# Kernel optimization log

Measured on AMD Instinct MI355X. Metric: run time of the kernel, lower is better.

Reference implementation:

```python
import jax, jax.numpy as jnp
import numpy as np

B, S, D, F, E, CAP = 4, 2048, 1024, 4096, 8, 320


def setup_inputs() -> dict:
    key = jax.random.key(0)
    k1, k2, k3, k4 = jax.random.split(key, 4)
    return {
        "hidden_states": jax.random.normal(k1, (B, S, D), dtype=jnp.float32),
        "router_w": jax.random.normal(k2, (D, E), dtype=jnp.float32) * 0.02,
        "wi": jax.random.normal(k3, (E, D, F), dtype=jnp.float32) * 0.02,
        "wo": jax.random.normal(k4, (E, F, D), dtype=jnp.float32) * 0.02,
    }


def reference(hidden_states, router_w, wi, wo):
    # ---- Router (Switch top-1 with per-sequence expert capacity) ----
    b, s, d = hidden_states.shape
    e = router_w.shape[1]
    logits = hidden_states.astype(jnp.float32) @ router_w          # [B,S,E]
    probs = jax.nn.softmax(logits, axis=-1)                        # [B,S,E]
    expert_idx = jnp.argmax(probs, axis=-1)                        # [B,S]
    onehot = jax.nn.one_hot(expert_idx, e, dtype=jnp.int32)        # [B,S,E]
    priority = jnp.cumsum(onehot, axis=1)                          # cumsum over seq dim (dim=-2)
    keep = onehot * (priority <= CAP).astype(jnp.int32)            # capacity-masked router_mask

    # slot of each token within its chosen expert (0-based)
    slot = jnp.take_along_axis(priority, expert_idx[..., None], axis=-1)[..., 0] - 1  # [B,S]
    valid = slot < CAP                                             # dropped tokens exceed capacity
    slot_sc = jnp.where(valid, slot, CAP)                          # out-of-range -> dropped by scatter

    b_ar = jnp.broadcast_to(jnp.arange(b)[:, None], (b, s))
    s_ar = jnp.broadcast_to(jnp.arange(s)[None, :], (b, s))
    dispatch = jnp.zeros((b, e, CAP), jnp.int32).at[b_ar, expert_idx, slot_sc].set(
        s_ar.astype(jnp.int32), mode="drop")                       # [B,E,CAP] token index per slot
    slot_used = jnp.zeros((b, e, CAP), bool).at[b_ar, expert_idx, slot_sc].set(
        valid, mode="drop")                                        # [B,E,CAP]

    # ---- Dispatch: gather tokens into [B,E,CAP,D] ----
    xg = jax.vmap(lambda xb, ib: xb[ib])(hidden_states, dispatch)  # [B,E,CAP,D]

    # ---- Per-expert dense FFN (grouped GEMM) ----
    hg = jax.nn.relu(jnp.einsum("becd,edf->becf", xg, wi))         # [B,E,CAP,F]
    yg = jnp.einsum("becf,efd->becd", hg, wo)                      # [B,E,CAP,D]

    # ---- Combine: scatter expert outputs back; unrouted tokens keep input ----
    idx_back = jnp.where(slot_used, dispatch, s)                   # out-of-range -> dropped
    next_states = jax.vmap(
        lambda xb, ib, yb: xb.at[ib.reshape(-1)].set(yb.reshape(-1, d), mode="drop")
    )(hidden_states, idx_back, yg)                                 # [B,S,D]

    max_prob = jnp.max(probs, axis=-1, keepdims=True)              # [B,S,1]
    out = max_prob * next_states
    expert_index_out = jnp.argmax(keep, axis=-1)                   # [B,S] (0 for dropped tokens)
    return out, logits, expert_index_out
```

## Files before the change

kernel.cpp:

```cpp
#include <hip/hip_runtime.h>
#include <hip/hip_bf16.h>
#include <stdint.h>

#define B_ 4
#define S_ 2048
#define D_ 1024
#define F_ 4096
#define E_ 8
#define CAP_ 320
#define BS_ (B_*S_)
#define MPE 1280

typedef unsigned short u16;
typedef __attribute__((ext_vector_type(8))) short bf16x8;
typedef __attribute__((ext_vector_type(4))) float f32x4;
typedef __attribute__((ext_vector_type(4))) unsigned short u16x4;
typedef __attribute__((ext_vector_type(8))) unsigned short u16x8;

__device__ __forceinline__ u16 f2bf(float f) {
  union { float f; uint32_t u; } v; v.f = f;
  uint32_t r = (v.u + 0x7FFFu + ((v.u >> 16) & 1u)) >> 16;
  return (u16)r;
}

__device__ __forceinline__ void gload16(const void* g, void* l) {
  __builtin_amdgcn_global_load_lds(
      (const __attribute__((address_space(1))) uint32_t*)g,
      (__attribute__((address_space(3))) uint32_t*)l, 16, 0, 0);
}

__device__ __forceinline__ void transpose_block(
    const float* __restrict__ W, u16* __restrict__ WT,
    const int K, const int N, const int bid, void* ldsraw)
{
  float (*tile)[65] = (float(*)[65])ldsraw;
  const int tk = K >> 7, tn = N >> 6;
  const int e = bid / (tk * tn), r = bid % (tk * tn);
  const int k0 = (r / tn) << 7, n0 = (r % tn) << 6;
  const float* We = W + (size_t)e * K * N;
  u16* WTe = WT + (size_t)e * N * K;
  const int t = threadIdx.x;
  const int fr = t >> 2, c0 = (t & 3) * 16;
#pragma unroll
  for (int j = 0; j < 4; ++j) {
    const float4 v = *(const float4*)(We + (size_t)(k0 + fr) * N + n0 + c0 + j * 4);
    tile[fr][c0 + j*4 + 0] = v.x; tile[fr][c0 + j*4 + 1] = v.y;
    tile[fr][c0 + j*4 + 2] = v.z; tile[fr][c0 + j*4 + 3] = v.w;
  }
  __syncthreads();
  const int nr = t >> 3, kk0 = (t & 7) * 16;
  u16x8 o0, o1;
#pragma unroll
  for (int j = 0; j < 8; ++j) o0[j] = f2bf(tile[kk0 + j][nr]);
#pragma unroll
  for (int j = 0; j < 8; ++j) o1[j] = f2bf(tile[kk0 + 8 + j][nr]);
  u16* dst = WTe + (size_t)(n0 + nr) * K + k0 + kk0;
  *(u16x8*)dst = o0;
  *(u16x8*)(dst + 8) = o1;
}

__global__ __launch_bounds__(512) void transpose_kernel(
    const float* __restrict__ W, u16* __restrict__ WT, const int K, const int N)
{
  __shared__ __align__(16) float tile[128][65];
  transpose_block(W, WT, K, N, blockIdx.x, (void*)tile);
}

__global__ __launch_bounds__(512) void prep_kernel(
    const float* __restrict__ hs, const float* __restrict__ rw,
    const float* __restrict__ wi, u16* __restrict__ wT,
    float* __restrict__ logits, float* __restrict__ maxp,
    int* __restrict__ eidx, const int twiT)
{
  __shared__ __align__(16) float tile[128][65];
  if ((int)blockIdx.x < twiT) {
    transpose_block(wi, wT, D_, F_, blockIdx.x, (void*)tile);
    return;
  }
  const int wv = threadIdx.x >> 6, l = threadIdx.x & 63;
  const int token = (blockIdx.x - twiT) * 8 + wv;
  const float* row = hs + (size_t)token * D_;
  const float4* rw4 = (const float4*)rw;

  double acc0=0, acc1=0, acc2=0, acc3=0, acc4=0, acc5=0, acc6=0, acc7=0;
#pragma unroll
  for (int j = 0; j < 4; ++j) {
    const int d4 = l + j * 64;
    const float4 v = ((const float4*)row)[d4];
#pragma unroll
    for (int c = 0; c < 4; ++c) {
      const int d = d4 * 4 + c;
      const float x = (&v.x)[c];
      const float4 w0 = rw4[d * 2];
      const float4 w1 = rw4[d * 2 + 1];
      acc0 += (double)x * (double)w0.x;
      acc1 += (double)x * (double)w0.y;
      acc2 += (double)x * (double)w0.z;
      acc3 += (double)x * (double)w0.w;
      acc4 += (double)x * (double)w1.x;
      acc5 += (double)x * (double)w1.y;
      acc6 += (double)x * (double)w1.z;
      acc7 += (double)x * (double)w1.w;
    }
  }
  double acc[E_] = {acc0, acc1, acc2, acc3, acc4, acc5, acc6, acc7};
#pragma unroll
  for (int e = 0; e < E_; ++e) {
#pragma unroll
    for (int off = 32; off; off >>= 1)
      acc[e] += __shfl_xor(acc[e], off);
  }
  if (l == 0) {
    float lg[E_];
#pragma unroll
    for (int e = 0; e < E_; ++e) lg[e] = (float)acc[e];
    float lmax = lg[0]; int am = 0;
#pragma unroll
    for (int e = 1; e < E_; ++e) { if (lg[e] > lmax) { lmax = lg[e]; am = e; } }
    float sum = 0.f;
#pragma unroll
    for (int e = 0; e < E_; ++e) sum += expf(lg[e] - lmax);
#pragma unroll
    for (int e = 0; e < E_; ++e) logits[(size_t)token * E_ + e] = lg[e];
    maxp[token] = 1.0f / sum;
    eidx[token] = am;
  }
}

__global__ __launch_bounds__(256) void scan_kernel(
    const int* __restrict__ eidx, int* __restrict__ tok,
    float* __restrict__ eout, const float* __restrict__ hs,
    const float* __restrict__ maxp, float* __restrict__ out)
{
  const int b = blockIdx.x >> 3, e = blockIdx.x & 7;
  __shared__ int wsum[4];
  const int tid = threadIdx.x, wv = tid >> 6, l = tid & 63;
  for (int i = tid; i < CAP_; i += 256) tok[(b * E_ + e) * CAP_ + i] = -1;
  __syncthreads();
  int base = 0;
  for (int ch = 0; ch < S_ / 256; ++ch) {
    const int s = ch * 256 + tid;
    const bool p = (eidx[b * S_ + s] == e);
    const unsigned long long m = __ballot(p);
    const int lp = __popcll(m & ((1ULL << l) - 1ULL));
    if (l == 0) wsum[wv] = __popcll(m);
    __syncthreads();
    int pre = 0, tot = 0;
#pragma unroll
    for (int w = 0; w < 4; ++w) { if (w < wv) pre += wsum[w]; tot += wsum[w]; }
    if (p) {
      const int rank = base + pre + lp;
      if (rank < CAP_) {
        tok[(b * E_ + e) * CAP_ + rank] = s;
        eout[b * S_ + s] = (float)e;
      } else {
        eout[b * S_ + s] = 0.0f;
        const float mp = maxp[b * S_ + s];
        const float4* src = (const float4*)(hs + (size_t)(b * S_ + s) * D_);
        float4* dst = (float4*)(out + (size_t)(b * S_ + s) * D_);
        for (int j = 0; j < D_ / 4; ++j) {
          const float4 vv = src[j];
          float4 o; o.x = vv.x * mp; o.y = vv.y * mp; o.z = vv.z * mp; o.w = vv.w * mp;
          dst[j] = o;
        }
      }
    }
    base += tot;
    __syncthreads();
  }
}

__global__ __launch_bounds__(256) void gather_kernel(
    const float* __restrict__ hs, const int* __restrict__ tok,
    u16* __restrict__ Xg)
{
  const int bx = blockIdx.x;
  const int e = bx / MPE, r = bx % MPE;
  const int b = r / CAP_, c = r % CAP_;
  const int t = tok[(b * E_ + e) * CAP_ + c];
  const int d = threadIdx.x * 4;
  u16x4 o;
  if (t >= 0) {
    const float4 vv = *(const float4*)(hs + ((size_t)(b * S_ + t)) * D_ + d);
    o[0] = f2bf(vv.x); o[1] = f2bf(vv.y); o[2] = f2bf(vv.z); o[3] = f2bf(vv.w);
  } else {
    o[0] = 0; o[1] = 0; o[2] = 0; o[3] = 0;
  }
  *(u16x4*)(Xg + (size_t)bx * D_ + d) = o;
}

#define BAR() __builtin_amdgcn_s_barrier()
#define VMW(n) asm volatile("s_waitcnt vmcnt(" #n ")" ::: "memory")

__global__ __launch_bounds__(512, 2) void moe_g1(
    const u16* __restrict__ Aall, const u16* __restrict__ Btall,
    u16* __restrict__ hgout, const int gemm_blocks,
    const float* __restrict__ Wtr, u16* __restrict__ WTtr)
{
  __shared__ __align__(16) u16 lds[49152];

#define LDA(p, h) (lds + (p) * 8192 + (h) * 4096)
#define LDB(p, h) (lds + 16384 + (p) * 16384 + (h) * 8192)

  if ((int)blockIdx.x >= gemm_blocks) {
    transpose_block(Wtr, WTtr, F_, D_, blockIdx.x - gemm_blocks, (void*)lds);
    return;
  }
  const int K = D_, NT = K >> 6, N = F_;
  const int cpx = gemm_blocks >> 3;
  const int bid = blockIdx.x;
  const int swzb = (bid & 7) * cpx + (bid >> 3);
  const int e = swzb / 160, rem = swzb % 160;
  const int m0 = (rem % 10) * 128, n0 = (rem / 10) * 256;

  const u16* Ae = Aall + (size_t)e * MPE * K;
  const u16* Be = Btall + (size_t)e * N * K;

  const int tid = threadIdx.x;
  const int wv = tid >> 6, l = tid & 63;
  const int wr = wv >> 2, wc = wv & 3;
  const int lr = l & 15, lk = l >> 4;
  const int rswz = ((lr >> 3) & 1) << 4;
  const int gs0 = tid ^ (((tid >> 5) & 1) << 1);
  const size_t goffB = (size_t)((gs0 >> 2) & 127) * K + (size_t)((gs0 & 3) * 8);
  const size_t goffA = (size_t)((gs0 >> 2) & 63) * K
                     + (size_t)(((gs0 >> 8) & 1) * 32) + (size_t)((gs0 & 3) * 8);
  const int dwoff = wv * 512;

  const u16* pA0 = Ae + (size_t)m0 * K;
  const u16* pA1 = Ae + (size_t)(m0 + 64) * K;
  const u16* pB0 = Be + (size_t)n0 * K;
  const u16* pB1 = Be + (size_t)(n0 + 128) * K;

  f32x4 acc[4][4];
#pragma unroll
  for (int i = 0; i < 4; ++i)
#pragma unroll
    for (int j = 0; j < 4; ++j) acc[i][j] = (f32x4){0.f, 0.f, 0.f, 0.f};

  bf16x8 faA[2], faB[2], fb[8];

#define STAGE_A1(dhalf, rb, tt) \
    gload16((rb) + goffA + (size_t)((tt) * 64), (dhalf) + dwoff)

#define STAGE_B1(dhalf, rb, tt) do {                                       \
    const u16* s_ = (rb) + goffB + (size_t)((tt) * 64);                    \
    gload16(s_,      (dhalf) + dwoff);                                     \
    gload16(s_ + 32, (dhalf) + 4096 + dwoff);                              \
  } while (0)

#define READ_AQ1(q, p, fa_) do {                                           \
    _Pragma("unroll")                                                      \
    for (int kk = 0; kk < 2; ++kk)                                         \
      fa_[kk] = *(const bf16x8*)&LDA(p, wr)                                \
          [(kk*64 + (q)*16 + lr)*32 + ((lk*8) ^ rswz)];                    \
  } while (0)

#define READ_B_ALL1(p) do {                                                \
    _Pragma("unroll")                                                      \
    for (int nf = 0; nf < 4; ++nf)                                         \
      _Pragma("unroll")                                                    \
      for (int kk = 0; kk < 2; ++kk)                                       \
        fb[nf*2+kk] = *(const bf16x8*)&LDB(p, wc>>1)                       \
            [(kk*128 + (wc&1)*64 + (nf>>1)*32 + (nf&1)*16 + lr)*32         \
             + ((lk*8) ^ rswz)];                                           \
  } while (0)

#define MFMA_P1(q, fa_) do {                                               \
    __builtin_amdgcn_s_setprio(1);                                         \
    _Pragma("unroll")                                                      \
    for (int nf = 0; nf < 4; ++nf)                                         \
      _Pragma("unroll")                                                    \
      for (int kk = 0; kk < 2; ++kk)                                       \
        acc[q][nf] = __builtin_amdgcn_mfma_f32_16x16x32_bf16(              \
            fa_[kk], fb[nf*2+kk], acc[q][nf], 0, 0, 0);                    \
    __builtin_amdgcn_s_setprio(0);                                         \
  } while (0)

#define DO_T1(p, pn, tc) do {                                              \
    READ_AQ1(1, p, faB);                                                   \
    if ((tc) + 1 < NT) { STAGE_A1(LDA(pn,0), pA0, (tc)+1);                 \
                         STAGE_A1(LDA(pn,1), pA1, (tc)+1); }               \
    MFMA_P1(0, faA);                                                       \
    READ_AQ1(2, p, faA);                                                   \
    MFMA_P1(1, faB);                                                       \
    BAR();                                                                 \
    READ_AQ1(3, p, faB);                                                   \
    if ((tc) + 2 < NT) { STAGE_B1(LDB(p,0), pB0, (tc)+2);                  \
                         STAGE_B1(LDB(p,1), pB1, (tc)+2); }                \
    MFMA_P1(2, faA);                                                       \
    MFMA_P1(3, faB);                                                       \
    if ((tc) >= NT - 2) VMW(0); else VMW(4);                               \
    BAR();                                                                 \
    if ((tc) + 1 < NT) { READ_B_ALL1(pn); READ_AQ1(0, pn, faA); }          \
  } while (0)

  STAGE_A1(LDA(0,0), pA0, 0);
  STAGE_A1(LDA(0,1), pA1, 0);
  STAGE_B1(LDB(0,0), pB0, 0);
  STAGE_B1(LDB(0,1), pB1, 0);
  STAGE_B1(LDB(1,0), pB0, 1);
  STAGE_B1(LDB(1,1), pB1, 1);
  VMW(4); BAR();
  READ_B_ALL1(0); READ_AQ1(0, 0, faA);

  for (int t = 0; t < NT; t += 2) {
    DO_T1(0, 1, t);
    DO_T1(1, 0, t + 1);
  }

#pragma unroll
  for (int i = 0; i < 4; ++i) {
#pragma unroll
    for (int r = 0; r < 4; ++r) {
      const int grow = m0 + wr * 64 + i * 16 + lk * 4 + r;
      u16* hrow = hgout + ((size_t)e * MPE + grow) * (size_t)N + n0 + wc * 64;
#pragma unroll
      for (int j = 0; j < 4; ++j)
        hrow[j * 16 + lr] = f2bf(fmaxf(acc[i][j][r], 0.0f));
    }
  }
#undef LDA
#undef LDB
#undef STAGE_A1
#undef STAGE_B1
#undef READ_AQ1
#undef READ_B_ALL1
#undef MFMA_P1
#undef DO_T1
}

__global__ __launch_bounds__(512, 2) void moe_g2(
    const u16* __restrict__ Aall, const u16* __restrict__ Btall,
    float* __restrict__ out, const int* __restrict__ tok,
    const float* __restrict__ maxp)
{
  __shared__ __align__(16) u16 lds[2][2][2][8192];

  const int K = F_, NT = K >> 6, N = D_;
  const int gemm_blocks = 160, cpx = gemm_blocks >> 3;
  const int bid = blockIdx.x;
  const int swzb = (bid & 7) * cpx + (bid >> 3);
  const int e = swzb / 20, rem = swzb % 20;
  const int m0 = (rem % 5) * 256, n0 = (rem / 5) * 256;

  const u16* Ae = Aall + (size_t)e * MPE * K;
  const u16* Be = Btall + (size_t)e * N * K;

  const int tid = threadIdx.x;
  const int wv = tid >> 6, l = tid & 63;
  const int wr = wv >> 2, wc = wv & 3;
  const int lr = l & 15, lk = l >> 4;
  const int rswz = ((lr >> 3) & 1) << 4;
  const int gs0 = tid ^ (((tid >> 5) & 1) << 1);
  const size_t goff = (size_t)((gs0 >> 2) & 127) * K + (size_t)((gs0 & 3) * 8);
  const int dwoff = wv * 512;

  const u16* pA0 = Ae + (size_t)m0 * K;
  const u16* pA1 = Ae + (size_t)(m0 + 128) * K;
  const u16* pB0 = Be + (size_t)n0 * K;
  const u16* pB1 = Be + (size_t)(n0 + 128) * K;

  f32x4 acc[8][4];
#pragma unroll
  for (int i = 0; i < 8; ++i)
#pragma unroll
    for (int j = 0; j < 4; ++j) acc[i][j] = (f32x4){0.f, 0.f, 0.f, 0.f};

  bf16x8 faA[4], faB[4], fb[8];

#define LDSH(p, ab, h) (&lds[p][ab][h][0])

#define STAGE2(dhalf, rb, tt) do {                                         \
    const u16* s_ = (rb) + goff + (size_t)((tt) * 64);                     \
    gload16(s_,      (dhalf) + dwoff);                                     \
    gload16(s_ + 32, (dhalf) + 4096 + dwoff);                              \
  } while (0)

#define READ_AQ2(q, p, fa_) do {                                           \
    _Pragma("unroll")                                                      \
    for (int mf = 0; mf < 2; ++mf)                                         \
      _Pragma("unroll")                                                    \
      for (int kk = 0; kk < 2; ++kk)                                       \
        fa_[mf*2+kk] = *(const bf16x8*)&lds[p][0][wr]                      \
            [(kk*128 + (q)*32 + mf*16 + lr)*32 + ((lk*8) ^ rswz)];         \
  } while (0)

#define READ_B_ALL2(p) do {                                                \
    _Pragma("unroll")                                                      \
    for (int nf = 0; nf < 4; ++nf)                                         \
      _Pragma("unroll")                                                    \
      for (int kk = 0; kk < 2; ++kk)                                       \
        fb[nf*2+kk] = *(const bf16x8*)&lds[p][1][wc>>1]                    \
            [(kk*128 + (wc&1)*64 + (nf>>1)*32 + (nf&1)*16 + lr)*32         \
             + ((lk*8) ^ rswz)];                                           \
  } while (0)

#define MFMA_P2(q, fa_) do {                                               \
    __builtin_amdgcn_s_setprio(1);                                         \
    _Pragma("unroll")                                                      \
    for (int mf = 0; mf < 2; ++mf)                                         \
      _Pragma("unroll")                                                    \
      for (int nf = 0; nf < 4; ++nf)                                       \
        _Pragma("unroll")                                                  \
        for (int kk = 0; kk < 2; ++kk)                                     \
          acc[(q)*2+mf][nf] = __builtin_amdgcn_mfma_f32_16x16x32_bf16(     \
              fa_[mf*2+kk], fb[nf*2+kk], acc[(q)*2+mf][nf], 0, 0, 0);      \
    __builtin_amdgcn_s_setprio(0);                                         \
  } while (0)

#define DO_T2(p, pn, tc) do {                                              \
    READ_AQ2(1, p, faB);                                                   \
    if ((tc) + 1 < NT) { STAGE2(LDSH(pn,0,0), pA0, (tc)+1);                \
                         STAGE2(LDSH(pn,0,1), pA1, (tc)+1); }              \
    MFMA_P2(0, faA);                                                       \
    READ_AQ2(2, p, faA);                                                   \
    MFMA_P2(1, faB);                                                       \
    BAR();                                                                 \
    READ_AQ2(3, p, faB);                                                   \
    if ((tc) + 2 < NT) { STAGE2(LDSH(p,1,0), pB0, (tc)+2);                 \
                         STAGE2(LDSH(p,1,1), pB1, (tc)+2); }               \
    MFMA_P2(2, faA);                                                       \
    MFMA_P2(3, faB);                                                       \
    if ((tc) >= NT - 2) VMW(0); else VMW(4);                               \
    BAR();                                                                 \
    if ((tc) + 1 < NT) { READ_B_ALL2(pn); READ_AQ2(0, pn, faA); }          \
  } while (0)

  STAGE2(LDSH(0,0,0), pA0, 0);
  STAGE2(LDSH(0,0,1), pA1, 0);
  STAGE2(LDSH(0,1,0), pB0, 0);
  STAGE2(LDSH(0,1,1), pB1, 0);
  STAGE2(LDSH(1,1,0), pB0, 1);
  STAGE2(LDSH(1,1,1), pB1, 1);
  VMW(4); BAR();
  READ_B_ALL2(0); READ_AQ2(0, 0, faA);

  for (int t = 0; t < NT; t += 2) {
    DO_T2(0, 1, t);
    DO_T2(1, 0, t + 1);
  }

#pragma unroll
  for (int i = 0; i < 8; ++i) {
#pragma unroll
    for (int r = 0; r < 4; ++r) {
      const int grow = m0 + wr * 128 + i * 16 + lk * 4 + r;
      const int b = grow / CAP_, c = grow % CAP_;
      const int t = tok[(b * E_ + e) * CAP_ + c];
      if (t >= 0) {
        const float sc = maxp[b * S_ + t];
        float* orow = out + ((size_t)(b * S_ + t)) * D_ + n0 + wc * 64;
#pragma unroll
        for (int j = 0; j < 4; ++j)
          orow[j * 16 + lr] = sc * acc[i][j][r];
      }
    }
  }
#undef LDSH
#undef STAGE2
#undef READ_AQ2
#undef READ_B_ALL2
#undef MFMA_P2
#undef DO_T2
}

extern "C" void kernel_launch(void* const* d_in, const int* in_sizes, int n_in,
                              void* d_out, int out_size, void* d_ws, size_t ws_size,
                              hipStream_t stream)
{
  const float* hs = (const float*)d_in[0];
  const float* rw = (const float*)d_in[1];
  const float* wi = (const float*)d_in[2];
  const float* wo = (const float*)d_in[3];

  float* out    = (float*)d_out;
  float* logits = out + (size_t)BS_ * D_;
  float* eout   = logits + (size_t)BS_ * E_;

  uint8_t* ws = (uint8_t*)d_ws;
  int*   tok  = (int*)(ws + 0);
  float* maxp = (float*)(ws + 40960);
  int*   eidx = (int*)(ws + 73728);
  u16*   Xg   = (u16*)(ws + 131072);
  u16*   hg   = (u16*)(ws + 21102592);
  u16*   wiT  = (u16*)(ws + 104988672);
  if (ws_size < 172097536ULL) return;
  const bool big = ws_size >= 239206400ULL;
  u16* woT = big ? (u16*)(ws + 172097536) : wiT;

  const int twiT = E_ * (D_ / 128) * (F_ / 64);
  const int twoT = E_ * (F_ / 128) * (D_ / 64);
  const int g1 = E_ * (MPE / 128) * (F_ / 256);
  const int g2 = 160;

  prep_kernel<<<twiT + BS_ / 8, 512, 0, stream>>>(
      hs, rw, wi, wiT, logits, maxp, eidx, twiT);
  scan_kernel<<<B_ * E_, 256, 0, stream>>>(eidx, tok, eout, hs, maxp, out);
  gather_kernel<<<E_ * MPE, 256, 0, stream>>>(hs, tok, Xg);

  if (big) {
    moe_g1<<<g1 + twoT, 512, 0, stream>>>(Xg, wiT, hg, g1, wo, woT);
  } else {
    moe_g1<<<g1, 512, 0, stream>>>(Xg, wiT, hg, g1, nullptr, nullptr);
    transpose_kernel<<<twoT, 512, 0, stream>>>(wo, woT, F_, D_);
  }
  moe_g2<<<g2, 512, 0, stream>>>(hg, woT, out, tok, maxp);
}
```

Before: 326.4 us.

## Single-buffer B tile in first grouped GEMM to cut LDS usage

The B operand in the first expert GEMM goes from double-buffered to a single LDS buffer, shrinking shared memory from 96KB to 64KB per block. The prefetch of B now runs one tile ahead instead of two. Each step waits for all global loads to finish and adds an extra barrier after the register reads from LDS. The aim is to lower LDS pressure, possibly to allow more resident blocks, at the cost of a shallower pipeline and extra synchronisation per K-step.

```diff
diff --git a/kernel.cpp b/kernel.cpp
--- a/kernel.cpp
+++ b/kernel.cpp
@@ -190,6 +190,7 @@
 }
 
 #define BAR() __builtin_amdgcn_s_barrier()
+#define LGKM0() asm volatile("s_waitcnt lgkmcnt(0)" ::: "memory")
 #define VMW(n) asm volatile("s_waitcnt vmcnt(" #n ")" ::: "memory")
 
 __global__ __launch_bounds__(512, 2) void moe_g1(
@@ -197,10 +198,10 @@
     u16* __restrict__ hgout, const int gemm_blocks,
     const float* __restrict__ Wtr, u16* __restrict__ WTtr)
 {
-  __shared__ __align__(16) u16 lds[49152];
+  __shared__ __align__(16) u16 lds[32768];
 
 #define LDA(p, h) (lds + (p) * 8192 + (h) * 4096)
-#define LDB(p, h) (lds + 16384 + (p) * 16384 + (h) * 8192)
+#define LDB(h)    (lds + 16384 + (h) * 8192)
 
   if ((int)blockIdx.x >= gemm_blocks) {
     transpose_block(Wtr, WTtr, F_, D_, blockIdx.x - gemm_blocks, (void*)lds);
@@ -256,12 +257,12 @@
           [(kk*64 + (q)*16 + lr)*32 + ((lk*8) ^ rswz)];                    \
   } while (0)
 
-#define READ_B_ALL1(p) do {                                                \
+#define READ_B_ALL1() do {                                                 \
     _Pragma("unroll")                                                      \
     for (int nf = 0; nf < 4; ++nf)                                         \
       _Pragma("unroll")                                                    \
       for (int kk = 0; kk < 2; ++kk)                                       \
-        fb[nf*2+kk] = *(const bf16x8*)&LDB(p, wc>>1)                       \
+        fb[nf*2+kk] = *(const bf16x8*)&LDB(wc>>1)                          \
             [(kk*128 + (wc&1)*64 + (nf>>1)*32 + (nf&1)*16 + lr)*32         \
              + ((lk*8) ^ rswz)];                                           \
   } while (0)
@@ -278,31 +279,33 @@
   } while (0)
 
 #define DO_T1(p, pn, tc) do {                                              \
+    if ((tc) + 1 < NT) {                                                   \
+      STAGE_A1(LDA(pn,0), pA0, (tc)+1);                                    \
+      STAGE_A1(LDA(pn,1), pA1, (tc)+1);                                    \
+      STAGE_B1(LDB(0), pB0, (tc)+1);                                       \
+      STAGE_B1(LDB(1), pB1, (tc)+1);                                       \
+    }                                                                      \
     READ_AQ1(1, p, faB);                                                   \
-    if ((tc) + 1 < NT) { STAGE_A1(LDA(pn,0), pA0, (tc)+1);                 \
-                         STAGE_A1(LDA(pn,1), pA1, (tc)+1); }               \
     MFMA_P1(0, faA);                                                       \
     READ_AQ1(2, p, faA);                                                   \
     MFMA_P1(1, faB);                                                       \
-    BAR();                                                                 \
     READ_AQ1(3, p, faB);                                                   \
-    if ((tc) + 2 < NT) { STAGE_B1(LDB(p,0), pB0, (tc)+2);                  \
-                         STAGE_B1(LDB(p,1), pB1, (tc)+2); }                \
     MFMA_P1(2, faA);                                                       \
     MFMA_P1(3, faB);                                                       \
-    if ((tc) >= NT - 2) VMW(0); else VMW(4);                               \
+    VMW(0);                                                                \
     BAR();                                                                 \
-    if ((tc) + 1 < NT) { READ_B_ALL1(pn); READ_AQ1(0, pn, faA); }          \
+    if ((tc) + 1 < NT) { READ_B_ALL1(); READ_AQ1(0, pn, faA); }            \
+    LGKM0();                                                               \
+    BAR();                                                                 \
   } while (0)
 
   STAGE_A1(LDA(0,0), pA0, 0);
   STAGE_A1(LDA(0,1), pA1, 0);
-  STAGE_B1(LDB(0,0), pB0, 0);
-  STAGE_B1(LDB(0,1), pB1, 0);
-  STAGE_B1(LDB(1,0), pB0, 1);
-  STAGE_B1(LDB(1,1), pB1, 1);
-  VMW(4); BAR();
-  READ_B_ALL1(0); READ_AQ1(0, 0, faA);
+  STAGE_B1(LDB(0), pB0, 0);
+  STAGE_B1(LDB(1), pB1, 0);
+  VMW(0); BAR();
+  READ_B_ALL1(); READ_AQ1(0, 0, faA);
+  LGKM0(); BAR();
 
   for (int t = 0; t < NT; t += 2) {
     DO_T1(0, 1, t);
```

Result: slower. 343.7 us (+5.3%).

## Fold wo transpose tiles into GEMM1 blocks via register prefetch and epilogue

Applied to the files above, without the earlier changes.

Each GEMM1 block now loads one wo transpose tile into registers before its main loop and writes it transposed through LDS after the epilogue. The remaining transpose tiles run as separate trailing blocks indexed by absolute block id. This shrinks the grid from g1+twoT to twoT blocks and hides the transpose loads behind GEMM compute. The cost is extra register pressure in the GEMM blocks, which already run under launch bounds of 512 threads and 2 blocks, so occupancy or spilling could suffer.

```diff
diff --git a/kernel.cpp b/kernel.cpp
--- a/kernel.cpp
+++ b/kernel.cpp
@@ -203,7 +203,7 @@
 #define LDB(p, h) (lds + 16384 + (p) * 16384 + (h) * 8192)
 
   if ((int)blockIdx.x >= gemm_blocks) {
-    transpose_block(Wtr, WTtr, F_, D_, blockIdx.x - gemm_blocks, (void*)lds);
+    transpose_block(Wtr, WTtr, F_, D_, blockIdx.x, (void*)lds);
     return;
   }
   const int K = D_, NT = K >> 6, N = F_;
@@ -239,6 +239,19 @@
     for (int j = 0; j < 4; ++j) acc[i][j] = (f32x4){0.f, 0.f, 0.f, 0.f};
 
   bf16x8 faA[2], faB[2], fb[8];
+
+  float4 tw0, tw1, tw2, tw3;
+  const int twid = bid;
+  if (Wtr) {
+    const int tr = twid & 511;
+    const int tk0 = (tr >> 4) << 7, tn0 = (tr & 15) << 6;
+    const float* Wb = Wtr + (size_t)(twid >> 9) * F_ * D_
+        + (size_t)(tk0 + (tid >> 4)) * D_ + tn0 + (tid & 15) * 4;
+    tw0 = *(const float4*)(Wb);
+    tw1 = *(const float4*)(Wb + 32 * D_);
+    tw2 = *(const float4*)(Wb + 64 * D_);
+    tw3 = *(const float4*)(Wb + 96 * D_);
+  }
 
 #define STAGE_A1(dhalf, rb, tt) \
     gload16((rb) + goffA + (size_t)((tt) * 64), (dhalf) + dwoff)
@@ -320,6 +333,33 @@
         hrow[j * 16 + lr] = f2bf(fmaxf(acc[i][j][r], 0.0f));
     }
   }
+
+  if (Wtr) {
+    BAR();
+    float (*tile)[65] = (float(*)[65])lds;
+    const int fr_ = tid >> 4, c0_ = (tid & 15) * 4;
+    float4 twv[4] = {tw0, tw1, tw2, tw3};
+#pragma unroll
+    for (int j = 0; j < 4; ++j) {
+      tile[j * 32 + fr_][c0_ + 0] = twv[j].x;
+      tile[j * 32 + fr_][c0_ + 1] = twv[j].y;
+      tile[j * 32 + fr_][c0_ + 2] = twv[j].z;
+      tile[j * 32 + fr_][c0_ + 3] = twv[j].w;
+    }
+    __syncthreads();
+    const int tr = twid & 511;
+    const int tk0 = (tr >> 4) << 7, tn0 = (tr & 15) << 6;
+    u16* WTe = WTtr + (size_t)(twid >> 9) * F_ * D_;
+    const int nr = tid >> 3, kk0 = (tid & 7) * 16;
+    u16x8 o0, o1;
+#pragma unroll
+    for (int j = 0; j < 8; ++j) o0[j] = f2bf(tile[kk0 + j][nr]);
+#pragma unroll
+    for (int j = 0; j < 8; ++j) o1[j] = f2bf(tile[kk0 + 8 + j][nr]);
+    u16* dst = WTe + (size_t)(tn0 + nr) * F_ + tk0 + kk0;
+    *(u16x8*)dst = o0;
+    *(u16x8*)(dst + 8) = o1;
+  }
 #undef LDA
 #undef LDB
 #undef STAGE_A1
@@ -500,7 +540,7 @@
   gather_kernel<<<E_ * MPE, 256, 0, stream>>>(hs, tok, Xg);
 
   if (big) {
-    moe_g1<<<g1 + twoT, 512, 0, stream>>>(Xg, wiT, hg, g1, wo, woT);
+    moe_g1<<<g1 + (twoT - g1), 512, 0, stream>>>(Xg, wiT, hg, g1, wo, woT);
   } else {
     moe_g1<<<g1, 512, 0, stream>>>(Xg, wiT, hg, g1, nullptr, nullptr);
     transpose_kernel<<<twoT, 512, 0, stream>>>(wo, woT, F_, D_);
```

Result: no change. 328.7 us (+0.7%).
